# Kernel tuning notes

Hardware: AMD Instinct MI355X
Metric: run time of the kernel (lower is better)

Reference implementation:

```python
import jax, jax.numpy as jnp
import numpy as np
from jax import lax

NUM_BLOCKS = 8
BLOCK = 4  # hidden_size 32 // num_blocks 8
LAMBDA = 0.01  # sparsity_threshold
BN_EPS = 1e-5


def _bn(x, gamma, beta):
    # training-mode BatchNorm2d over (N, H, W) per channel
    mean = jnp.mean(x, axis=(0, 2, 3), keepdims=True)
    var = jnp.var(x, axis=(0, 2, 3), keepdims=True)
    return gamma[None, :, None, None] * (x - mean) * lax.rsqrt(var + BN_EPS) + beta[None, :, None, None]


def _softshrink(x, lam):
    return jnp.where(x > lam, x - lam, jnp.where(x < -lam, x + lam, jnp.zeros_like(x)))


def _afno(x, w1, b1, w2, b2):
    # AFNO2D_channelfirst: rfft2 -> block-diagonal complex 2-layer MLP -> softshrink
    # -> multiply with original spectrum -> irfft2 -> residual add
    B, C, H, W = x.shape
    bias = x
    xf = jnp.fft.rfft2(x, axes=(2, 3), norm="ortho")          # [B, C, H, W//2+1] complex
    orig = xf
    Wf = xf.shape[-1]
    xb = xf.reshape(B, NUM_BLOCKS, BLOCK, H, Wf)
    xr, xi = jnp.real(xb), jnp.imag(xb)
    # layer 1 (complex block matmul + bias + ReLU)
    o1r = jax.nn.relu(jnp.einsum('bkihw,kio->bkohw', xr, w1[0])
                      - jnp.einsum('bkihw,kio->bkohw', xi, w1[1])
                      + b1[0][None, :, :, None, None])
    o1i = jax.nn.relu(jnp.einsum('bkihw,kio->bkohw', xi, w1[0])
                      + jnp.einsum('bkihw,kio->bkohw', xr, w1[1])
                      + b1[1][None, :, :, None, None])
    # layer 2
    o2r = (jnp.einsum('bkihw,kio->bkohw', o1r, w2[0])
           - jnp.einsum('bkihw,kio->bkohw', o1i, w2[1])
           + b2[0][None, :, :, None, None])
    o2i = (jnp.einsum('bkihw,kio->bkohw', o1i, w2[0])
           + jnp.einsum('bkihw,kio->bkohw', o1r, w2[1])
           + b2[1][None, :, :, None, None])
    o2r = _softshrink(o2r, LAMBDA)
    o2i = _softshrink(o2i, LAMBDA)
    z = (o2r + 1j * o2i).reshape(B, C, H, Wf)
    z = z * orig                                              # spectral gating by original spectrum
    out = jnp.fft.irfft2(z, s=(H, W), axes=(2, 3), norm="ortho")
    return out + bias


def setup_inputs() -> dict:
    key = jax.random.key(0)
    ks = jax.random.split(key, 6)
    return {
        "x": jax.random.normal(ks[0], (4, 32, 512, 512), jnp.float32),
        "conv_w": jax.random.normal(ks[1], (32, 32, 3, 3), jnp.float32) * 0.05,
        "conv_b": jnp.zeros((32,), jnp.float32),
        "bn1_gamma": jnp.ones((32,), jnp.float32),
        "bn1_beta": jnp.zeros((32,), jnp.float32),
        "w1": jax.random.normal(ks[2], (2, NUM_BLOCKS, BLOCK, BLOCK), jnp.float32) * 0.02,
        "b1": jax.random.normal(ks[3], (2, NUM_BLOCKS, BLOCK), jnp.float32) * 0.02,
        "w2": jax.random.normal(ks[4], (2, NUM_BLOCKS, BLOCK, BLOCK), jnp.float32) * 0.02,
        "b2": jax.random.normal(ks[5], (2, NUM_BLOCKS, BLOCK), jnp.float32) * 0.02,
        "bn2_gamma": jnp.ones((32,), jnp.float32),
        "bn2_beta": jnp.zeros((32,), jnp.float32),
    }


def reference(x, conv_w, conv_b, bn1_gamma, bn1_beta, w1, b1, w2, b2, bn2_gamma, bn2_beta):
    # conv1 = Conv3x3(norm=True, act=True): conv 3x3 pad 1 + BN + ReLU
    y = lax.conv_general_dilated(x, conv_w, (1, 1), ((1, 1), (1, 1)),
                                 dimension_numbers=('NCHW', 'OIHW', 'NCHW'))
    y = y + conv_b[None, :, None, None]
    y = jax.nn.relu(_bn(y, bn1_gamma, bn1_beta))
    fo = _afno(y, w1, b1, w2, b2)
    fo = _bn(fo, bn2_gamma, bn2_beta)
    return jax.nn.relu(y + fo)
```

## Files before the change

### kernel.cpp

```cpp
#include <hip/hip_runtime.h>

#define WF 257
#define LAM 0.01f
#define ROWL 588
#define LP(i) ((i) + (((i)>>4)<<1) + (((i)>>6)<<1))

typedef __attribute__((ext_vector_type(8))) short short8;
typedef __attribute__((ext_vector_type(4))) float f32x4;

__device__ __forceinline__ ushort f2bf(float f){
    unsigned u = __float_as_uint(f);
    unsigned r = (u + 0x7fffu + ((u >> 16) & 1u)) >> 16;
    return (ushort)r;
}
__device__ __forceinline__ float bf2f(ushort u){ return __uint_as_float((uint)u << 16); }
__device__ __forceinline__ uint packbf(float a, float b){
    return (uint)f2bf(a) | ((uint)f2bf(b) << 16);
}
__device__ __forceinline__ float2 unpackbf(uint u){
    return make_float2(__uint_as_float(u << 16), __uint_as_float(u & 0xffff0000u));
}

__device__ __forceinline__ float2 cmul(float2 a, float2 b){
    return make_float2(a.x*b.x - a.y*b.y, a.x*b.y + a.y*b.x);
}
__device__ __forceinline__ float2 cadd(float2 a, float2 b){ return make_float2(a.x+b.x, a.y+b.y); }
__device__ __forceinline__ float2 csub(float2 a, float2 b){ return make_float2(a.x-b.x, a.y-b.y); }

template<int NTHREADS>
__device__ __forceinline__ void ld_tw(float2* tw, const float2* __restrict__ twg, int tid){
    for (int t = tid; t < 256; t += NTHREADS)
        ((float4*)tw)[t] = ((const float4*)twg)[t];
}

template<bool INV>
__device__ __forceinline__ float2 twz(const float2* tw, int idx){
    float2 w = tw[idx];
    if (INV) w.y = -w.y;
    return w;
}

template<bool INV>
__device__ __forceinline__ void dft8(float2 v[8]) {
    const float R = 0.70710678118654752f;
    float2 y0=v[0], y1=v[4], y2=v[2], y3=v[6], y4=v[1], y5=v[5], y6=v[3], y7=v[7];
    float2 t;
    t=y1; y1=csub(y0,t); y0=cadd(y0,t);
    t=y3; y3=csub(y2,t); y2=cadd(y2,t);
    t=y5; y5=csub(y4,t); y4=cadd(y4,t);
    t=y7; y7=csub(y6,t); y6=cadd(y6,t);
    t=y2; y2=csub(y0,t); y0=cadd(y0,t);
    t = INV ? make_float2(-y3.y, y3.x) : make_float2(y3.y, -y3.x);
    y3=csub(y1,t); y1=cadd(y1,t);
    t=y6; y6=csub(y4,t); y4=cadd(y4,t);
    t = INV ? make_float2(-y7.y, y7.x) : make_float2(y7.y, -y7.x);
    y7=csub(y5,t); y5=cadd(y5,t);
    t=y4; y4=csub(y0,t); y0=cadd(y0,t);
    { float2 w8 = INV ? make_float2(R, R) : make_float2(R,-R);
      t=cmul(y5,w8); y5=csub(y1,t); y1=cadd(y1,t); }
    t = INV ? make_float2(-y6.y, y6.x) : make_float2(y6.y, -y6.x);
    y6=csub(y2,t); y2=cadd(y2,t);
    { float2 w8 = INV ? make_float2(-R, R) : make_float2(-R,-R);
      t=cmul(y7,w8); y7=csub(y3,t); y3=cadd(y3,t); }
    v[0]=y0; v[1]=y1; v[2]=y2; v[3]=y3; v[4]=y4; v[5]=y5; v[6]=y6; v[7]=y7;
}

__device__ __forceinline__ void oct_write(float2* drow, int l, const float2 v[8]){
    float4* p = (float4*)(drow + LP(8*l));
    p[0]=make_float4(v[0].x,v[0].y,v[1].x,v[1].y);
    p[1]=make_float4(v[2].x,v[2].y,v[3].x,v[3].y);
    p[2]=make_float4(v[4].x,v[4].y,v[5].x,v[5].y);
    p[3]=make_float4(v[6].x,v[6].y,v[7].x,v[7].y);
}

__device__ __forceinline__ void oct_gather(const float2* drow, int o0, float2 v[8]){
    const float2* b = drow + LP(o0);
    #pragma unroll
    for (int q = 0; q < 8; ++q) v[q] = b[74*q];
}

template<int NROWS, int NTHREADS, bool INV>
__device__ __forceinline__ void fft_st12(float2* d, const float2* tw, int tid)
{
    __syncthreads();
    #pragma unroll
    for (int rep = 0; rep < (NROWS*64)/NTHREADS; ++rep){
        int slot = rep*NTHREADS + tid;
        int row = slot>>6, l = slot&63;
        int a = l&7, m = l>>3;
        float2* b = d + row*ROWL + 74*m + a;
        float2 v[8];
        v[0] = b[0];
        v[1] = cmul(b[8],  twz<INV>(tw, 8*a));
        v[2] = cmul(b[18], twz<INV>(tw, 16*a));
        v[3] = cmul(b[26], twz<INV>(tw, 24*a));
        v[4] = cmul(b[36], twz<INV>(tw, 32*a));
        v[5] = cmul(b[44], twz<INV>(tw, 40*a));
        v[6] = cmul(b[54], twz<INV>(tw, 48*a));
        v[7] = cmul(b[62], twz<INV>(tw, 56*a));
        dft8<INV>(v);
        b[0]=v[0]; b[8]=v[1]; b[18]=v[2]; b[26]=v[3]; b[36]=v[4]; b[44]=v[5]; b[54]=v[6]; b[62]=v[7];
    }
    __syncthreads();
    #pragma unroll
    for (int rep = 0; rep < (NROWS*64)/NTHREADS; ++rep){
        int slot = rep*NTHREADS + tid;
        int row = slot>>6, l = slot&63;
        float2* b = d + row*ROWL + l + 2*(l>>4);
        float2 v[8];
        v[0] = b[0];
        #pragma unroll
        for (int q = 1; q < 8; ++q)
            v[q] = cmul(b[74*q], twz<INV>(tw, (l*q)&511));
        dft8<INV>(v);
        #pragma unroll
        for (int q = 0; q < 8; ++q) b[74*q] = v[q];
    }
    __syncthreads();
}

__global__ void k_twiddle(float2* __restrict__ twg){
    int t = blockIdx.x*256 + threadIdx.x;
    if (t < 512) {
        float s, c;
        sincosf((float)t * (-6.2831853071795864769f/512.0f), &s, &c);
        twg[t] = make_float2(c, s);
    }
}

__global__ void k_wprep(const float* __restrict__ w, ushort* __restrict__ wtp){
    int i = blockIdx.x*256 + threadIdx.x;
    if (i < 9216) {
        int j = i & 7, l = (i>>3) & 63, m = (i>>9) & 1, tap = i >> 10;
        int co = m*16 + (l & 15), ci = ((l>>4)&3)*8 + j;
        wtp[i] = f2bf(w[(co*32 + ci)*9 + tap]);
    }
}

__global__ __launch_bounds__(256) void k_transpose(const float* __restrict__ x, ushort* __restrict__ xt){
    __shared__ ushort tl[64][36];
    const int tid = threadIdx.x;
    const int w0 = blockIdx.x*64, h = blockIdx.y, b = blockIdx.z;
    #pragma unroll
    for (int it = 0; it < 8; ++it) {
        int i = it*256 + tid, c = i >> 6, ww = i & 63;
        tl[ww][c] = f2bf(x[(((size_t)b*32 + c)*512 + h)*512 + w0 + ww]);
    }
    __syncthreads();
    const int ww = tid >> 2, c0 = (tid & 3) * 8;
    uint4 v;
    v.x = *(const uint*)&tl[ww][c0+0];
    v.y = *(const uint*)&tl[ww][c0+2];
    v.z = *(const uint*)&tl[ww][c0+4];
    v.w = *(const uint*)&tl[ww][c0+6];
    *(uint4*)(xt + ((((size_t)b*512 + h)*512 + w0 + ww)*32 + c0)) = v;
}

__global__ __launch_bounds__(256) void k_conv_mfma(
    const ushort* __restrict__ xt, const ushort* __restrict__ wtp,
    const float* __restrict__ bias, ushort* __restrict__ out, float* __restrict__ stats)
{
    __shared__ float sred[64];
    const int tid = threadIdx.x;
    const int wid = tid >> 6, lane = tid & 63;
    const int h = blockIdx.y*4 + wid;
    const int w0 = blockIdx.x*64;
    const int b = blockIdx.z;

    short8 wa[9][2];
    #pragma unroll
    for (int tap = 0; tap < 9; ++tap)
        #pragma unroll
        for (int m = 0; m < 2; ++m)
            wa[tap][m] = *reinterpret_cast<const short8*>(wtp + ((tap*2 + m)*64 + lane)*8);

    f32x4 acc[2][4];
    #pragma unroll
    for (int m = 0; m < 2; ++m)
        #pragma unroll
        for (int n = 0; n < 4; ++n)
            acc[m][n] = (f32x4){0.f, 0.f, 0.f, 0.f};

    const int c0 = ((lane >> 4) & 3) * 8;
    const int pw = w0 + (lane & 15);
    const size_t ibase = (size_t)b * 512 * 512;

    #pragma unroll
    for (int dy = -1; dy <= 1; ++dy) {
        const int hh = h + dy;
        const bool hok = (unsigned)hh < 512u;
        #pragma unroll
        for (int dx = -1; dx <= 1; ++dx) {
            const int tap = (dy+1)*3 + (dx+1);
            short8 bfr[4];
            #pragma unroll
            for (int n = 0; n < 4; ++n) {
                const int ww = pw + n*16 + dx;
                short8 v = {0,0,0,0,0,0,0,0};
                if (hok && (unsigned)ww < 512u)
                    v = *reinterpret_cast<const short8*>(xt + ((ibase + (size_t)hh*512 + ww)*32 + c0));
                bfr[n] = v;
            }
            #pragma unroll
            for (int m = 0; m < 2; ++m)
                #pragma unroll
                for (int n = 0; n < 4; ++n)
                    acc[m][n] = __builtin_amdgcn_mfma_f32_16x16x32_bf16(wa[tap][m], bfr[n], acc[m][n], 0, 0, 0);
        }
    }

    if (tid < 64) sred[tid] = 0.f;
    __syncthreads();

    float bv[2][4];
    #pragma unroll
    for (int m = 0; m < 2; ++m)
        #pragma unroll
        for (int r = 0; r < 4; ++r)
            bv[m][r] = bias[m*16 + ((lane>>4)&3)*4 + r];

    float s8[8], q8[8];
    #pragma unroll
    for (int i = 0; i < 8; ++i) { s8[i] = 0.f; q8[i] = 0.f; }

    #pragma unroll
    for (int m = 0; m < 2; ++m) {
        #pragma unroll
        for (int n = 0; n < 4; ++n) {
            #pragma unroll
            for (int r = 0; r < 4; ++r) {
                const int co = m*16 + ((lane>>4)&3)*4 + r;
                const int ww = w0 + n*16 + (lane & 15);
                float val = acc[m][n][r] + bv[m][r];
                out[(((size_t)b*32 + co)*512 + h)*512 + ww] = f2bf(val);
                s8[m*4+r] += val;
                q8[m*4+r] += val*val;
            }
        }
    }
    #pragma unroll
    for (int i = 0; i < 8; ++i) {
        #pragma unroll
        for (int off = 1; off < 16; off <<= 1) {
            s8[i] += __shfl_xor(s8[i], off, 64);
            q8[i] += __shfl_xor(q8[i], off, 64);
        }
    }
    if ((lane & 15) == 0) {
        #pragma unroll
        for (int m = 0; m < 2; ++m)
            #pragma unroll
            for (int r = 0; r < 4; ++r) {
                const int co = m*16 + ((lane>>4)&3)*4 + r;
                atomicAdd(&sred[co], s8[m*4+r]);
                atomicAdd(&sred[32+co], q8[m*4+r]);
            }
    }
    __syncthreads();
    if (tid < 64) {
        int bin = (blockIdx.y*8 + blockIdx.x + blockIdx.z) & 63;
        atomicAdd(&stats[bin*64 + tid], sred[tid]);
    }
}

__global__ void k_finalize(const float* __restrict__ stats, int nbins, const float* __restrict__ g,
                           const float* __restrict__ bta, float* __restrict__ bnp)
{
    int c = threadIdx.x;
    if (c < 32) {
        float s = 0.f, q = 0.f;
        for (int i = 0; i < nbins; ++i) { s += stats[i*64 + c]; q += stats[i*64 + 32 + c]; }
        const float inv_n = 1.f/1048576.f;
        float mean = s * inv_n;
        float var  = q * inv_n - mean*mean;
        float sc = g[c] * rsqrtf(var + 1e-5f);
        bnp[c] = sc;
        bnp[32+c] = bta[c] - mean*sc;
    }
}

__global__ void k_finalize2(const float* __restrict__ ystats, const float* __restrict__ sstats,
                            const float* __restrict__ g, const float* __restrict__ bta,
                            float* __restrict__ bnp2)
{
    int c = threadIdx.x;
    if (c < 32) {
        float Sy = 0.f, Sy2 = 0.f, Sgg = 0.f, Sgu = 0.f, Sg0 = 0.f;
        for (int i = 0; i < 64; ++i){ Sy  += ystats[i*64 + c]; Sy2 += ystats[i*64 + 32 + c]; }
        for (int i = 0; i < 32; ++i){ Sgg += sstats[i*96 + c]; Sgu += sstats[i*96 + 32 + c]; Sg0 += sstats[i*96 + 64 + c]; }
        const float inv_n = 1.f/1048576.f;
        float Sfo  = Sg0 + Sy;
        float Sfo2 = Sgg*(1.f/512.f) + Sgu*(2.f/512.f) + Sy2;
        float mean = Sfo*inv_n;
        float var  = Sfo2*inv_n - mean*mean;
        float sc = g[c]*rsqrtf(var + 1e-5f);
        bnp2[c] = sc;
        bnp2[32+c] = bta[c] - mean*sc;
    }
}

__global__ __launch_bounds__(512) void k_rowfft_fwd(
    const ushort* __restrict__ cvo, const float* __restrict__ bnp,
    const float2* __restrict__ twg, uint* __restrict__ spec, float* __restrict__ ystats)
{
    __shared__ float2 tw[512];
    __shared__ float2 d[8*ROWL];
    __shared__ float red[16];
    const int tid = threadIdx.x;
    const int h0 = blockIdx.x * 16;
    const int bc = blockIdx.y;
    const int c = bc & 31;
    ld_tw<512>(tw, twg, tid);
    const float s1 = bnp[c], t1 = bnp[32+c];
    const int row = tid >> 6, l = tid & 63;
    const int o0 = ((l&7)<<3) | (l>>3);
    const ushort* rp0 = cvo + ((size_t)bc*512 + h0 + 2*row)*512 + o0;
    const ushort* rp1 = rp0 + 512;
    float ls = 0.f, lsq = 0.f;
    float2 v[8];
    #pragma unroll
    for (int q = 0; q < 8; ++q) {
        float y0 = fmaxf(fmaf(bf2f(rp0[64*q]), s1, t1), 0.f);
        float y1 = fmaxf(fmaf(bf2f(rp1[64*q]), s1, t1), 0.f);
        ls += y0 + y1; lsq += y0*y0 + y1*y1;
        v[q] = make_float2(y0, y1);
    }
    dft8<false>(v);
    oct_write(d + row*ROWL, l, v);
    fft_st12<8,512,false>(d, tw, tid);
    for (int i = tid; i < 8*WF; i += 512) {
        int p = i & 7, w = i >> 3;
        float2 Z  = d[p*ROWL + LP(w)];
        float2 Zm = d[p*ROWL + LP((512 - w) & 511)];
        float x1r = 0.5f*(Z.x + Zm.x), x1i = 0.5f*(Z.y - Zm.y);
        float x2r = 0.5f*(Z.y + Zm.y), x2i = 0.5f*(Zm.x - Z.x);
        uint2 pk;
        pk.x = packbf(x1r, x1i);
        pk.y = packbf(x2r, x2i);
        *(uint2*)(spec + ((size_t)bc*WF + w)*512 + h0 + 2*p) = pk;
    }
    #pragma unroll
    for (int off = 32; off; off >>= 1){ ls += __shfl_down(ls, off, 64); lsq += __shfl_down(lsq, off, 64); }
    if ((tid & 63) == 0){ red[(tid>>6)*2] = ls; red[(tid>>6)*2+1] = lsq; }
    __syncthreads();
    if (tid == 0) {
        float a = 0.f, b = 0.f;
        #pragma unroll
        for (int i = 0; i < 8; ++i){ a += red[i*2]; b += red[i*2+1]; }
        int bin = blockIdx.x & 63;
        atomicAdd(&ystats[bin*64 + c], a);
        atomicAdd(&ystats[bin*64 + 32 + c], b);
    }
}

__global__ __launch_bounds__(256) void k_colfft(uint* __restrict__ spec,
    const float* __restrict__ w1, const float* __restrict__ b1,
    const float* __restrict__ w2, const float* __restrict__ b2,
    const float2* __restrict__ twg, float* __restrict__ sstats)
{
    __shared__ float2 tw[512];
    __shared__ float2 d[4*ROWL];
    __shared__ float wl[80];
    __shared__ float red[4][12];
    const int tid = threadIdx.x;
    const int w = blockIdx.x;
    const int k = blockIdx.y;
    const int b = blockIdx.z;
    ld_tw<256>(tw, twg, tid);
    if (tid < 16) {
        wl[tid]      = w1[k*16 + tid];
        wl[16 + tid] = w1[128 + k*16 + tid];
        wl[32 + tid] = w2[k*16 + tid];
        wl[48 + tid] = w2[128 + k*16 + tid];
    } else if (tid < 20) {
        int o = tid - 16;
        wl[64 + o] = b1[k*4 + o];
        wl[68 + o] = b1[32 + k*4 + o];
        wl[72 + o] = b2[k*4 + o];
        wl[76 + o] = b2[32 + k*4 + o];
    }
    const size_t base0 = ((size_t)(b*32 + k*4)*WF + w) * 512;
    const int cc0 = tid >> 6, l = tid & 63;
    const int o0 = ((l&7)<<3) | (l>>3);
    {
        const uint* sp = spec + base0 + (size_t)cc0*(WF*512) + o0;
        float2 v[8];
        #pragma unroll
        for (int q = 0; q < 8; ++q) v[q] = unpackbf(sp[64*q]);
        dft8<false>(v);
        oct_write(d + cc0*ROWL, l, v);
    }
    fft_st12<4,256,false>(d, tw, tid);
    #pragma unroll
    for (int rep = 0; rep < 2; ++rep) {
        const int ph = LP(rep*256 + tid);
        float xr[4], xi[4];
        #pragma unroll
        for (int i = 0; i < 4; ++i) {
            float2 vv = d[i*ROWL + ph];
            xr[i] = vv.x * (1.f/512.f);
            xi[i] = vv.y * (1.f/512.f);
        }
        float o1r[4], o1i[4];
        #pragma unroll
        for (int o = 0; o < 4; ++o) {
            float sr = wl[64+o], si = wl[68+o];
            #pragma unroll
            for (int i = 0; i < 4; ++i) {
                float wr = wl[i*4+o], wi = wl[16 + i*4+o];
                sr += xr[i]*wr - xi[i]*wi;
                si += xi[i]*wr + xr[i]*wi;
            }
            o1r[o] = fmaxf(sr, 0.f);
            o1i[o] = fmaxf(si, 0.f);
        }
        #pragma unroll
        for (int o = 0; o < 4; ++o) {
            float sr = wl[72+o], si = wl[76+o];
            #pragma unroll
            for (int i = 0; i < 4; ++i) {
                float wr = wl[32 + i*4+o], wi = wl[48 + i*4+o];
                sr += o1r[i]*wr - o1i[i]*wi;
                si += o1i[i]*wr + o1r[i]*wi;
            }
            sr = (sr > LAM) ? sr - LAM : ((sr < -LAM) ? sr + LAM : 0.f);
            si = (si > LAM) ? si - LAM : ((si < -LAM) ? si + LAM : 0.f);
            d[o*ROWL + ph] = make_float2(sr*xr[o] - si*xi[o], sr*xi[o] + si*xr[o]);
        }
    }
    __syncthreads();
    {
        float2 v[8];
        oct_gather(d + cc0*ROWL, o0, v);
        dft8<true>(v);
        __syncthreads();
        oct_write(d + cc0*ROWL, l, v);
    }
    fft_st12<4,256,true>(d, tw, tid);
    const bool edge = (w == 0) || (w == 256);
    float fl[12];
    #pragma unroll
    for (int i = 0; i < 12; ++i) fl[i] = 0.f;
    #pragma unroll
    for (int cc = 0; cc < 4; ++cc) {
        uint2 up = *(const uint2*)(spec + base0 + (size_t)cc*(WF*512) + 2*tid);
        float2 u0 = unpackbf(up.x), u1 = unpackbf(up.y);
        float4 vv = *(const float4*)(d + cc*ROWL + LP(2*tid));
        uint2 gp;
        gp.x = packbf(vv.x, vv.y);
        gp.y = packbf(vv.z, vv.w);
        *(uint2*)(spec + base0 + (size_t)cc*(WF*512) + 2*tid) = gp;
        float2 g0 = unpackbf(gp.x), g1 = unpackbf(gp.y);
        if (edge) {
            fl[cc]   += g0.x*g0.x + g1.x*g1.x;
            fl[4+cc] += g0.x*u0.x + g1.x*u1.x;
            if (w == 0) fl[8+cc] += g0.x + g1.x;
        } else {
            fl[cc]   += 2.f*(g0.x*g0.x + g0.y*g0.y + g1.x*g1.x + g1.y*g1.y);
            fl[4+cc] += 2.f*(g0.x*u0.x + g0.y*u0.y + g1.x*u1.x + g1.y*u1.y);
        }
    }
    #pragma unroll
    for (int i = 0; i < 12; ++i)
        #pragma unroll
        for (int off = 32; off; off >>= 1)
            fl[i] += __shfl_down(fl[i], off, 64);
    const int wid = tid >> 6, lane = tid & 63;
    if (lane == 0)
        #pragma unroll
        for (int i = 0; i < 12; ++i) red[wid][i] = fl[i];
    __syncthreads();
    if (tid < 12) {
        float v = red[0][tid] + red[1][tid] + red[2][tid] + red[3][tid];
        int type = tid >> 2, cc = tid & 3;
        if (type < 2 || w == 0) {
            int bin = (w + b*8 + k) & 31;
            atomicAdd(&sstats[bin*96 + type*32 + k*4 + cc], v);
        }
    }
}

__global__ __launch_bounds__(512) void k_rowfft_inv(
    const uint* __restrict__ spec, const ushort* __restrict__ cvo,
    const float* __restrict__ bnp, const float* __restrict__ bnp2,
    const float2* __restrict__ twg, float* __restrict__ out)
{
    __shared__ float2 tw[512];
    __shared__ float2 d[8*ROWL];
    const int tid = threadIdx.x;
    const int h0 = blockIdx.x * 16;
    const int bc = blockIdx.y;
    const int c = bc & 31;
    ld_tw<512>(tw, twg, tid);
    for (int i = tid; i < 8*WF; i += 512) {
        int p = i & 7, w = i >> 3;
        uint2 pk = *(const uint2*)(spec + ((size_t)bc*WF + w)*512 + h0 + 2*p);
        float2 X1 = unpackbf(pk.x), X2 = unpackbf(pk.y);
        if (w == 0 || w == 256) { X1.y = 0.f; X2.y = 0.f; }
        d[p*ROWL + LP(w)] = make_float2(X1.x - X2.y, X1.y + X2.x);
        if ((unsigned)(w - 1) < 255u)
            d[p*ROWL + LP(512 - w)] = make_float2(X1.x + X2.y, X2.x - X1.y);
    }
    __syncthreads();
    const int row = tid >> 6, l = tid & 63;
    const int o0 = ((l&7)<<3) | (l>>3);
    {
        float2 v[8];
        oct_gather(d + row*ROWL, o0, v);
        dft8<true>(v);
        __syncthreads();
        oct_write(d + row*ROWL, l, v);
    }
    fft_st12<8,512,true>(d, tw, tid);
    const float s1 = bnp[c],  t1 = bnp[32+c];
    const float s2 = bnp2[c], t2 = bnp2[32+c];
    #pragma unroll
    for (int p = 0; p < 8; ++p) {
        float2 v = d[p*ROWL + LP(tid)];
        size_t g0 = ((size_t)bc*512 + h0 + 2*p)*512 + tid;
        float y0 = fmaxf(fmaf(bf2f(cvo[g0]), s1, t1), 0.f);
        float fo0 = fmaf(v.x, (1.f/512.f), y0);
        out[g0] = fmaxf(y0 + fmaf(fo0, s2, t2), 0.f);
        float y1 = fmaxf(fmaf(bf2f(cvo[g0 + 512]), s1, t1), 0.f);
        float fo1 = fmaf(v.y, (1.f/512.f), y1);
        out[g0 + 512] = fmaxf(y1 + fmaf(fo1, s2, t2), 0.f);
    }
}

extern "C" void kernel_launch(void* const* d_in, const int* in_sizes, int n_in,
                              void* d_out, int out_size, void* d_ws, size_t ws_size,
                              hipStream_t stream)
{
    const float* x      = (const float*)d_in[0];
    const float* conv_w = (const float*)d_in[1];
    const float* conv_b = (const float*)d_in[2];
    const float* bn1g   = (const float*)d_in[3];
    const float* bn1b   = (const float*)d_in[4];
    const float* w1     = (const float*)d_in[5];
    const float* b1     = (const float*)d_in[6];
    const float* w2     = (const float*)d_in[7];
    const float* b2     = (const float*)d_in[8];
    const float* bn2g   = (const float*)d_in[9];
    const float* bn2b   = (const float*)d_in[10];
    float* out = (float*)d_out;

    char* ws = (char*)d_ws;
    uint*   spec  = (uint*)ws;
    ushort* xt    = (ushort*)ws;
    ushort* cvo   = (ushort*)(ws + 67371008);
    ushort* wtp   = (ushort*)(ws + 67371008 + 67108864);
    float*  stats = (float*)(ws + 67371008 + 67108864 + 18432);
    float* stats1 = stats;
    float* ystats = stats + 4096;
    float* sstats = stats + 8192;
    float* bnp1   = stats + 11264;
    float* bnp2   = stats + 11328;
    float2* twg   = (float2*)(stats + 11392);

    hipMemsetAsync(stats, 0, 11264*sizeof(float), stream);
    k_twiddle<<<2, 256, 0, stream>>>(twg);
    k_wprep<<<36, 256, 0, stream>>>(conv_w, wtp);
    k_transpose<<<dim3(8,512,4), 256, 0, stream>>>(x, xt);
    k_conv_mfma<<<dim3(8,128,4), 256, 0, stream>>>(xt, wtp, conv_b, cvo, stats1);
    k_finalize<<<1, 64, 0, stream>>>(stats1, 64, bn1g, bn1b, bnp1);
    k_rowfft_fwd<<<dim3(32,128), 512, 0, stream>>>(cvo, bnp1, twg, spec, ystats);
    k_colfft<<<dim3(257,8,4), 256, 0, stream>>>(spec, w1, b1, w2, b2, twg, sstats);
    k_finalize2<<<1, 64, 0, stream>>>(ystats, sstats, bn2g, bn2b, bnp2);
    k_rowfft_inv<<<dim3(32,128), 512, 0, stream>>>(spec, cvo, bnp1, bnp2, twg, out);
}
```

Baseline: 374.8 us.

## Make each wave own one FFT row and replace block barriers with wave barriers

```diff
diff --git a/kernel.cpp b/kernel.cpp
--- a/kernel.cpp
+++ b/kernel.cpp
@@ -4,6 +4,8 @@
 #define LAM 0.01f
 #define ROWL 588
 #define LP(i) ((i) + (((i)>>4)<<1) + (((i)>>6)<<1))
+
+#define WSYNC() do { asm volatile("" ::: "memory"); __builtin_amdgcn_wave_barrier(); asm volatile("" ::: "memory"); } while(0)
 
 typedef __attribute__((ext_vector_type(8))) short short8;
 typedef __attribute__((ext_vector_type(4))) float f32x4;
@@ -79,16 +81,13 @@
     for (int q = 0; q < 8; ++q) v[q] = b[74*q];
 }
 
-template<int NROWS, int NTHREADS, bool INV>
-__device__ __forceinline__ void fft_st12(float2* d, const float2* tw, int tid)
-{
-    __syncthreads();
-    #pragma unroll
-    for (int rep = 0; rep < (NROWS*64)/NTHREADS; ++rep){
-        int slot = rep*NTHREADS + tid;
-        int row = slot>>6, l = slot&63;
+template<bool INV>
+__device__ __forceinline__ void fft_wave12(float2* drow, const float2* tw, int l)
+{
+    WSYNC();
+    {
         int a = l&7, m = l>>3;
-        float2* b = d + row*ROWL + 74*m + a;
+        float2* b = drow + 74*m + a;
         float2 v[8];
         v[0] = b[0];
         v[1] = cmul(b[8],  twz<INV>(tw, 8*a));
@@ -101,12 +100,9 @@
         dft8<INV>(v);
         b[0]=v[0]; b[8]=v[1]; b[18]=v[2]; b[26]=v[3]; b[36]=v[4]; b[44]=v[5]; b[54]=v[6]; b[62]=v[7];
     }
-    __syncthreads();
-    #pragma unroll
-    for (int rep = 0; rep < (NROWS*64)/NTHREADS; ++rep){
-        int slot = rep*NTHREADS + tid;
-        int row = slot>>6, l = slot&63;
-        float2* b = d + row*ROWL + l + 2*(l>>4);
+    WSYNC();
+    {
+        float2* b = drow + l + 2*(l>>4);
         float2 v[8];
         v[0] = b[0];
         #pragma unroll
@@ -116,7 +112,7 @@
         #pragma unroll
         for (int q = 0; q < 8; ++q) b[74*q] = v[q];
     }
-    __syncthreads();
+    WSYNC();
 }
 
 __global__ void k_twiddle(float2* __restrict__ twg){
@@ -305,15 +301,16 @@
 {
     __shared__ float2 tw[512];
     __shared__ float2 d[8*ROWL];
-    __shared__ float red[16];
     const int tid = threadIdx.x;
     const int h0 = blockIdx.x * 16;
     const int bc = blockIdx.y;
     const int c = bc & 31;
     ld_tw<512>(tw, twg, tid);
+    __syncthreads();
     const float s1 = bnp[c], t1 = bnp[32+c];
     const int row = tid >> 6, l = tid & 63;
     const int o0 = ((l&7)<<3) | (l>>3);
+    float2* drow = d + row*ROWL;
     const ushort* rp0 = cvo + ((size_t)bc*512 + h0 + 2*row)*512 + o0;
     const ushort* rp1 = rp0 + 512;
     float ls = 0.f, lsq = 0.f;
@@ -326,8 +323,9 @@
         v[q] = make_float2(y0, y1);
     }
     dft8<false>(v);
-    oct_write(d + row*ROWL, l, v);
-    fft_st12<8,512,false>(d, tw, tid);
+    oct_write(drow, l, v);
+    fft_wave12<false>(drow, tw, l);
+    __syncthreads();
     for (int i = tid; i < 8*WF; i += 512) {
         int p = i & 7, w = i >> 3;
         float2 Z  = d[p*ROWL + LP(w)];
@@ -341,15 +339,10 @@
     }
     #pragma unroll
     for (int off = 32; off; off >>= 1){ ls += __shfl_down(ls, off, 64); lsq += __shfl_down(lsq, off, 64); }
-    if ((tid & 63) == 0){ red[(tid>>6)*2] = ls; red[(tid>>6)*2+1] = lsq; }
-    __syncthreads();
-    if (tid == 0) {
-        float a = 0.f, b = 0.f;
-        #pragma unroll
-        for (int i = 0; i < 8; ++i){ a += red[i*2]; b += red[i*2+1]; }
-        int bin = blockIdx.x & 63;
-        atomicAdd(&ystats[bin*64 + c], a);
-        atomicAdd(&ystats[bin*64 + 32 + c], b);
+    if (l == 0) {
+        int bin = ((blockIdx.x << 3) + row) & 63;
+        atomicAdd(&ystats[bin*64 + c], ls);
+        atomicAdd(&ystats[bin*64 + 32 + c], lsq);
     }
 }
 
@@ -361,7 +354,6 @@
     __shared__ float2 tw[512];
     __shared__ float2 d[4*ROWL];
     __shared__ float wl[80];
-    __shared__ float red[4][12];
     const int tid = threadIdx.x;
     const int w = blockIdx.x;
     const int k = blockIdx.y;
@@ -379,18 +371,22 @@
         wl[72 + o] = b2[k*4 + o];
         wl[76 + o] = b2[32 + k*4 + o];
     }
+    __syncthreads();
     const size_t base0 = ((size_t)(b*32 + k*4)*WF + w) * 512;
-    const int cc0 = tid >> 6, l = tid & 63;
+    const int cc = tid >> 6, l = tid & 63;
     const int o0 = ((l&7)<<3) | (l>>3);
+    float2* drow = d + cc*ROWL;
+    const size_t cbase = base0 + (size_t)cc*(WF*512);
     {
-        const uint* sp = spec + base0 + (size_t)cc0*(WF*512) + o0;
+        const uint* sp = spec + cbase + o0;
         float2 v[8];
         #pragma unroll
         for (int q = 0; q < 8; ++q) v[q] = unpackbf(sp[64*q]);
         dft8<false>(v);
-        oct_write(d + cc0*ROWL, l, v);
-    }
-    fft_st12<4,256,false>(d, tw, tid);
+        oct_write(drow, l, v);
+    }
+    fft_wave12<false>(drow, tw, l);
+    __syncthreads();
     #pragma unroll
     for (int rep = 0; rep < 2; ++rep) {
         const int ph = LP(rep*256 + tid);
@@ -431,52 +427,45 @@
     __syncthreads();
     {
         float2 v[8];
-        oct_gather(d + cc0*ROWL, o0, v);
+        oct_gather(drow, o0, v);
         dft8<true>(v);
-        __syncthreads();
-        oct_write(d + cc0*ROWL, l, v);
-    }
-    fft_st12<4,256,true>(d, tw, tid);
+        WSYNC();
+        oct_write(drow, l, v);
+    }
+    fft_wave12<true>(drow, tw, l);
     const bool edge = (w == 0) || (w == 256);
-    float fl[12];
-    #pragma unroll
-    for (int i = 0; i < 12; ++i) fl[i] = 0.f;
-    #pragma unroll
-    for (int cc = 0; cc < 4; ++cc) {
-        uint2 up = *(const uint2*)(spec + base0 + (size_t)cc*(WF*512) + 2*tid);
+    float fgg = 0.f, fgu = 0.f, fg0 = 0.f;
+    #pragma unroll
+    for (int it = 0; it < 4; ++it) {
+        const int pos = it*64 + l;
+        uint2 up = *(const uint2*)(spec + cbase + 2*pos);
         float2 u0 = unpackbf(up.x), u1 = unpackbf(up.y);
-        float4 vv = *(const float4*)(d + cc*ROWL + LP(2*tid));
+        float4 vv = *(const float4*)(drow + LP(2*pos));
         uint2 gp;
         gp.x = packbf(vv.x, vv.y);
         gp.y = packbf(vv.z, vv.w);
-        *(uint2*)(spec + base0 + (size_t)cc*(WF*512) + 2*tid) = gp;
+        *(uint2*)(spec + cbase + 2*pos) = gp;
         float2 g0 = unpackbf(gp.x), g1 = unpackbf(gp.y);
         if (edge) {
-            fl[cc]   += g0.x*g0.x + g1.x*g1.x;
-            fl[4+cc] += g0.x*u0.x + g1.x*u1.x;
-            if (w == 0) fl[8+cc] += g0.x + g1.x;
+            fgg += g0.x*g0.x + g1.x*g1.x;
+            fgu += g0.x*u0.x + g1.x*u1.x;
+            if (w == 0) fg0 += g0.x + g1.x;
         } else {
-            fl[cc]   += 2.f*(g0.x*g0.x + g0.y*g0.y + g1.x*g1.x + g1.y*g1.y);
-            fl[4+cc] += 2.f*(g0.x*u0.x + g0.y*u0.y + g1.x*u1.x + g1.y*u1.y);
-        }
-    }
-    #pragma unroll
-    for (int i = 0; i < 12; ++i)
-        #pragma unroll
-        for (int off = 32; off; off >>= 1)
-            fl[i] += __shfl_down(fl[i], off, 64);
-    const int wid = tid >> 6, lane = tid & 63;
-    if (lane == 0)
-        #pragma unroll
-        for (int i = 0; i < 12; ++i) red[wid][i] = fl[i];
-    __syncthreads();
-    if (tid < 12) {
-        float v = red[0][tid] + red[1][tid] + red[2][tid] + red[3][tid];
-        int type = tid >> 2, cc = tid & 3;
-        if (type < 2 || w == 0) {
-            int bin = (w + b*8 + k) & 31;
-            atomicAdd(&sstats[bin*96 + type*32 + k*4 + cc], v);
-        }
+            fgg += 2.f*(g0.x*g0.x + g0.y*g0.y + g1.x*g1.x + g1.y*g1.y);
+            fgu += 2.f*(g0.x*u0.x + g0.y*u0.y + g1.x*u1.x + g1.y*u1.y);
+        }
+    }
+    #pragma unroll
+    for (int off = 32; off; off >>= 1){
+        fgg += __shfl_down(fgg, off, 64);
+        fgu += __shfl_down(fgu, off, 64);
+        fg0 += __shfl_down(fg0, off, 64);
+    }
+    if (l == 0) {
+        int bin = (w + b*8 + k) & 31;
+        atomicAdd(&sstats[bin*96 + k*4 + cc], fgg);
+        atomicAdd(&sstats[bin*96 + 32 + k*4 + cc], fgu);
+        if (w == 0) atomicAdd(&sstats[bin*96 + 64 + k*4 + cc], fg0);
     }
 }
 
@@ -504,26 +493,28 @@
     __syncthreads();
     const int row = tid >> 6, l = tid & 63;
     const int o0 = ((l&7)<<3) | (l>>3);
+    float2* drow = d + row*ROWL;
     {
         float2 v[8];
-        oct_gather(d + row*ROWL, o0, v);
+        oct_gather(drow, o0, v);
         dft8<true>(v);
-        __syncthreads();
-        oct_write(d + row*ROWL, l, v);
-    }
-    fft_st12<8,512,true>(d, tw, tid);
+        WSYNC();
+        oct_write(drow, l, v);
+    }
+    fft_wave12<true>(drow, tw, l);
     const float s1 = bnp[c],  t1 = bnp[32+c];
     const float s2 = bnp2[c], t2 = bnp2[32+c];
-    #pragma unroll
-    for (int p = 0; p < 8; ++p) {
-        float2 v = d[p*ROWL + LP(tid)];
-        size_t g0 = ((size_t)bc*512 + h0 + 2*p)*512 + tid;
-        float y0 = fmaxf(fmaf(bf2f(cvo[g0]), s1, t1), 0.f);
+    const size_t gbase = ((size_t)bc*512 + h0 + 2*row)*512;
+    #pragma unroll
+    for (int q = 0; q < 8; ++q) {
+        const int col = q*64 + l;
+        float2 v = drow[LP(col)];
+        float y0 = fmaxf(fmaf(bf2f(cvo[gbase + col]), s1, t1), 0.f);
         float fo0 = fmaf(v.x, (1.f/512.f), y0);
-        out[g0] = fmaxf(y0 + fmaf(fo0, s2, t2), 0.f);
-        float y1 = fmaxf(fmaf(bf2f(cvo[g0 + 512]), s1, t1), 0.f);
+        out[gbase + col] = fmaxf(y0 + fmaf(fo0, s2, t2), 0.f);
+        float y1 = fmaxf(fmaf(bf2f(cvo[gbase + 512 + col]), s1, t1), 0.f);
         float fo1 = fmaf(v.y, (1.f/512.f), y1);
-        out[g0 + 512] = fmaxf(y1 + fmaf(fo1, s2, t2), 0.f);
+        out[gbase + 512 + col] = fmaxf(y1 + fmaf(fo1, s2, t2), 0.f);
     }
 }
 
```

After: 350.1 us. 6.6% less time.
